# Performance work log

Hardware: AMD Instinct MI355X
Metric: run time of the kernel (lower is better)

## Reference

```python
import jax, jax.numpy as jnp
import numpy as np

L, N, D = 1024, 64, 1024  # seq_len, batch, d_model (= hidden)


def setup_inputs() -> dict:
    key = jax.random.key(0)
    k1, k2, k3 = jax.random.split(key, 3)
    x = jax.random.normal(k1, (L, N, D), dtype=jnp.float32)
    # flax OptimizedLSTMCell params: input kernel (no bias), recurrent kernel + bias,
    # gates packed as [i, f, g, o] along last dim.
    Wi = jax.random.normal(k2, (D, 4 * D), dtype=jnp.float32) / np.float32(np.sqrt(D))
    Wh = jax.random.normal(k3, (D, 4 * D), dtype=jnp.float32) / np.float32(np.sqrt(D))
    b = jnp.zeros((4 * D,), dtype=jnp.float32)
    return {"x": x, "Wi": Wi, "Wh": Wh, "b": b}


def reference(x, Wi, Wh, b):
    # x: [L, N, D]; scan LSTM cell over time axis 0 (matches nn.scan in_axes=0).
    d = Wh.shape[0]
    n = x.shape[1]
    # Input projections have no carry dependency: batch them in one big GEMM.
    xW = jnp.einsum('lnd,df->lnf', x, Wi)  # [L, N, 4D]

    def step(carry, xw_t):
        c, h = carry
        y = xw_t + h @ Wh + b  # [N, 4D]
        i, f, g, o = jnp.split(y, 4, axis=-1)
        i = jax.nn.sigmoid(i)
        f = jax.nn.sigmoid(f)
        g = jnp.tanh(g)
        o = jax.nn.sigmoid(o)
        c_new = f * c + i * g
        h_new = o * jnp.tanh(c_new)
        return (c_new, h_new), h_new

    c0 = jnp.zeros((n, d), dtype=x.dtype)
    h0 = jnp.zeros((n, d), dtype=x.dtype)
    _, hs = jax.lax.scan(step, (c0, h0), xW)
    return hs  # [L, N, D]
```

## Files before the change

kernel.cpp:

```cpp
#include <hip/hip_runtime.h>
#include <stdint.h>

#define LSEQ 1024
#define NB   64
#define DM   1024
#define FOURD 4096

typedef float f32x4 __attribute__((ext_vector_type(4)));
typedef short short8_t __attribute__((ext_vector_type(8)));
typedef __bf16 bf16x8 __attribute__((ext_vector_type(8)));

__device__ __forceinline__ unsigned short f2bf(float f) {
    unsigned int u = __builtin_bit_cast(unsigned int, f);
    u += 0x7fffu + ((u >> 16) & 1u);
    return (unsigned short)(u >> 16);
}

__device__ __forceinline__ f32x4 mfma16(short8_t a, short8_t b, f32x4 c) {
    return __builtin_amdgcn_mfma_f32_16x16x32_bf16(
        __builtin_bit_cast(bf16x8, a), __builtin_bit_cast(bf16x8, b), c, 0, 0, 0);
}

__global__ void init_ws_kernel(unsigned int* __restrict__ p, int n) {
    int i = blockIdx.x * blockDim.x + threadIdx.x;
    int stride = gridDim.x * blockDim.x;
    for (; i < n; i += stride) p[i] = 0u;
}

__global__ void convert_x_kernel(const float4* __restrict__ src, uint4* __restrict__ dst) {
    size_t i = (size_t)blockIdx.x * blockDim.x + threadIdx.x;
    float4 a = src[2 * i];
    float4 b = src[2 * i + 1];
    uint4 r;
    r.x = (unsigned)f2bf(a.x) | ((unsigned)f2bf(a.y) << 16);
    r.y = (unsigned)f2bf(a.z) | ((unsigned)f2bf(a.w) << 16);
    r.z = (unsigned)f2bf(b.x) | ((unsigned)f2bf(b.y) << 16);
    r.w = (unsigned)f2bf(b.z) | ((unsigned)f2bf(b.w) << 16);
    dst[i] = r;
}

__global__ void prep_w_kernel(const float* __restrict__ W,
                              unsigned short* __restrict__ wp) {
    const int fid = blockIdx.x * 256 + threadIdx.x;
    const int lane = fid & 63;
    const int kk = (fid >> 6) & 3;
    const int q  = (fid >> 8) & 3;
    const int ks = (fid >> 10) & 7;
    const int ug = fid >> 13;
    const int k0 = (ks << 7) + (kk << 5) + ((lane >> 4) << 3);
    const int col = (q << 10) + (ug << 4) + (lane & 15);
    short8_t v;
    #pragma unroll
    for (int j = 0; j < 8; ++j)
        v[j] = (short)f2bf(W[(size_t)(k0 + j) * FOURD + col]);
    *(short8_t*)(wp + ((size_t)fid << 3)) = v;
}

#define HL(arr, i, OFFS)                                                        \
    asm volatile("global_load_dwordx4 %0, %1, off offset:" OFFS " sc0 sc1"      \
                 : "=v"(arr[i]) : "v"(hap) : "memory")
#define XL(arr, i, OFFS)                                                        \
    asm volatile("global_load_dwordx4 %0, %1, off offset:" OFFS                 \
                 : "=v"(arr[i]) : "v"(xap) : "memory")
#define WAITV(NSTR)                                          \
    asm volatile("s_waitcnt vmcnt(" NSTR ")" ::: "memory");  \
    __builtin_amdgcn_sched_barrier(0)
#define WAITL()                                              \
    asm volatile("s_waitcnt lgkmcnt(0)" ::: "memory")
#define BARRIER()                                            \
    __builtin_amdgcn_s_barrier();                            \
    asm volatile("" ::: "memory")

__global__ __launch_bounds__(512)
__attribute__((amdgpu_waves_per_eu(2, 2)))
void lstm_scan_kernel(const unsigned short* __restrict__ wip,
                      const unsigned short* __restrict__ whp,
                      const float* __restrict__ bias,
                      const unsigned short* __restrict__ xb,
                      unsigned short* __restrict__ hbuf,
                      unsigned int* __restrict__ flags,
                      float* __restrict__ out)
{
    __shared__ float plds[8][4][16][20];
    const int tid = threadIdx.x;
    const int wg = blockIdx.x;
    const int rg = (wg & 7) >> 1;
    const int ug = (wg >> 3) | ((wg & 1) << 5);
    const int r0 = rg << 4, U0 = ug << 4;
    const int lane = tid & 63, ks = tid >> 6;
    const int la = lane & 15, kseg = lane >> 4;

    short8_t BI[4][4], BH[4][4];
    {
        const unsigned short* wb = wip + (((size_t)(ug << 3) + ks) << 13);
        const unsigned short* hb = whp + (((size_t)(ug << 3) + ks) << 13);
        #pragma unroll
        for (int q = 0; q < 4; ++q)
            #pragma unroll
            for (int kk = 0; kk < 4; ++kk) {
                const unsigned short* p1 = wb + ((((q << 2) + kk) << 6) + lane) * 8;
                const unsigned short* p2 = hb + ((((q << 2) + kk) << 6) + lane) * 8;
                asm volatile("global_load_dwordx4 %0, %1, off"
                             : "=v"(BI[q][kk]) : "v"(p1) : "memory");
                asm volatile("global_load_dwordx4 %0, %1, off"
                             : "=v"(BH[q][kk]) : "v"(p2) : "memory");
            }
        asm volatile("s_waitcnt vmcnt(0)" ::: "memory");
        __builtin_amdgcn_sched_barrier(0);
    }

    const int aoff = (r0 + la) * DM + (ks << 7) + (kseg << 3);

    const int er = tid >> 4, eu = tid & 15;
    const float bI = bias[U0 + eu], bF = bias[1024 + U0 + eu],
                bG = bias[2048 + U0 + eu], bO = bias[3072 + U0 + eu];
    float cst = 0.0f;
    unsigned int* myflag = flags + (rg << 6) + ug;
    const unsigned int* gfp = flags + (rg << 6) + lane;

    short8_t xf[4];
    {
        const unsigned short* xap = xb + aoff;
        XL(xf, 0, "0"); XL(xf, 1, "64"); XL(xf, 2, "128"); XL(xf, 3, "192");
        asm volatile("s_waitcnt vmcnt(0)" ::: "memory");
        __builtin_amdgcn_sched_barrier(0);
    }

    for (int t = 0; t < LSEQ; ++t) {
        if (t && tid < 64) {
            while (true) {
                unsigned int f = __hip_atomic_load(gfp, __ATOMIC_RELAXED,
                                                   __HIP_MEMORY_SCOPE_AGENT);
                if (__all((int)(f >= (unsigned)t))) break;
                __builtin_amdgcn_s_sleep(1);
            }
        }
        BARRIER();

        short8_t hf[4];
        {
            const unsigned short* hap =
                hbuf + (size_t)((t & 1) ^ 1) * (NB * DM) + aoff;
            HL(hf, 0, "0"); HL(hf, 1, "64"); HL(hf, 2, "128"); HL(hf, 3, "192");
        }
        WAITV("4");

        f32x4 acc[4];
        #pragma unroll
        for (int q = 0; q < 4; ++q) acc[q] = (f32x4){0.f, 0.f, 0.f, 0.f};
        #pragma unroll
        for (int kk = 0; kk < 4; ++kk)
            #pragma unroll
            for (int q = 0; q < 4; ++q)
                acc[q] = mfma16(xf[kk], BI[q][kk], acc[q]);

        WAITV("0");

        #pragma unroll
        for (int kk = 0; kk < 4; ++kk)
            #pragma unroll
            for (int q = 0; q < 4; ++q)
                acc[q] = mfma16(hf[kk], BH[q][kk], acc[q]);

        #pragma unroll
        for (int q = 0; q < 4; ++q)
            *(f32x4*)&plds[ks][q][la][kseg << 2] = acc[q];
        WAITL();
        BARRIER();

        float hv = 0.f, hn = 0.f;
        if (tid < 256) {
            float vi = bI, vf = bF, vg = bG, vo = bO;
            #pragma unroll
            for (int s = 0; s < 8; ++s) {
                vi += plds[s][0][eu][er];
                vf += plds[s][1][eu][er];
                vg += plds[s][2][eu][er];
                vo += plds[s][3][eu][er];
            }
            float gi = 1.0f / (1.0f + __expf(-vi));
            float gF = 1.0f / (1.0f + __expf(-vf));
            float gg = 1.0f - 2.0f / (__expf(2.0f * vg) + 1.0f);
            float go = 1.0f / (1.0f + __expf(-vo));
            cst = gF * cst + gi * gg;
            hv = go * (1.0f - 2.0f / (__expf(2.0f * cst) + 1.0f));
            hn = __shfl_xor(hv, 1);

            if (!(eu & 1)) {
                unsigned int hp = (unsigned)f2bf(hv) | ((unsigned)f2bf(hn) << 16);
                unsigned int* hw = (unsigned int*)(hbuf + (size_t)(t & 1) * (NB * DM)
                                                   + (size_t)(r0 + er) * DM + U0 + eu);
                asm volatile("global_store_dword %0, %1, off sc0 sc1"
                             :: "v"(hw), "v"(hp) : "memory");
            }
        }

        {
            const int tn = (t < LSEQ - 1) ? t + 1 : t;
            const unsigned short* xap = xb + (size_t)tn * (NB * DM) + aoff;
            XL(xf, 0, "0"); XL(xf, 1, "64"); XL(xf, 2, "128"); XL(xf, 3, "192");
        }
        WAITV("4");

        BARRIER();

        if (tid == 0)
            __hip_atomic_store(myflag, (unsigned)(t + 1), __ATOMIC_RELAXED,
                               __HIP_MEMORY_SCOPE_AGENT);

        if (tid < 256 && !(eu & 1))
            *(float2*)(out + ((size_t)(t * NB) + r0 + er) * DM + U0 + eu)
                = make_float2(hv, hn);
    }
}

#define HM(arr, i, kk) {                                        \
    short8_t b = *(const short8_t*)(bph + (kk) * 1024);         \
    if ((kk) & 1) acc1 = mfma16(arr[i], b, acc1);               \
    else          acc0 = mfma16(arr[i], b, acc0); }

__global__ __launch_bounds__(256)
void lstm_fallback_kernel(const float* __restrict__ x,
                          const float* __restrict__ Wi,
                          const float* __restrict__ Wh,
                          const float* __restrict__ bias,
                          unsigned short* __restrict__ hbuf,
                          unsigned int* __restrict__ flags,
                          float* __restrict__ out)
{
    __shared__ short Wlds[65536];
    __shared__ float ylds[32 * 33];
    __shared__ float blds[32];

    const int tid  = threadIdx.x;
    const int wgid = blockIdx.x;
    const int g    = wgid >> 7;
    const int ug   = wgid & 127;
    const int U0   = ug << 3;
    const int rowbase = g << 5;

    {
        const int c    = tid & 31;
        const int ct_  = c >> 4;
        const int lb   = c & 15;
        const int gcol = ((c >> 3) << 10) + U0 + (c & 7);
        for (int k = tid >> 5; k < 1024; k += 8) {
            const int lane_ = lb | (((k >> 3) & 3) << 4);
            const int sidx  = (ct_ * 32 + (k >> 5)) * 512 + lane_ * 8 + (k & 7);
            Wlds[sidx]         = (short)f2bf(Wi[(size_t)k * FOURD + gcol]);
            Wlds[sidx + 32768] = (short)f2bf(Wh[(size_t)k * FOURD + gcol]);
        }
        if (tid < 32) blds[tid] = bias[((tid >> 3) << 10) + U0 + (tid & 7)];
    }
    __syncthreads();

    const int lane = tid & 63;
    const int wv   = tid >> 6;
    const int rt   = wv >> 1;
    const int ct   = wv & 1;
    const int arow = rowbase + (rt << 4) + (lane & 15);
    const int kseg = (lane >> 4) << 3;
    const char* bpx = (const char*)Wlds + ct * 32768 + lane * 16;
    const char* bph = (const char*)Wlds + 65536 + ct * 32768 + lane * 16;

    const int er = tid >> 3;
    const int eu = tid & 7;
    const float bI = blds[eu], bF = blds[8 + eu], bG = blds[16 + eu], bO = blds[24 + eu];
    float cstate = 0.0f;
    unsigned int* gflags = flags + (g << 7);

    for (int t = 0; t < LSEQ; ++t) {
        f32x4 acc0 = {0.f, 0.f, 0.f, 0.f};
        f32x4 acc1 = {0.f, 0.f, 0.f, 0.f};

        {
            const float* ap = x + ((size_t)t * NB + arow) * DM + kseg;
            #pragma unroll 4
            for (int kk = 0; kk < 32; ++kk) {
                float4 lo = *(const float4*)(ap + kk * 32);
                float4 hi = *(const float4*)(ap + kk * 32 + 4);
                short8_t a;
                a[0] = (short)f2bf(lo.x); a[1] = (short)f2bf(lo.y);
                a[2] = (short)f2bf(lo.z); a[3] = (short)f2bf(lo.w);
                a[4] = (short)f2bf(hi.x); a[5] = (short)f2bf(hi.y);
                a[6] = (short)f2bf(hi.z); a[7] = (short)f2bf(hi.w);
                short8_t b = *(const short8_t*)(bpx + kk * 1024);
                if (kk & 1) acc1 = mfma16(a, b, acc1);
                else        acc0 = mfma16(a, b, acc0);
            }
        }

        if (t && wv == 0) {
            const unsigned int* fp = gflags + (lane << 1);
            while (true) {
                unsigned int f0 = __hip_atomic_load(fp,     __ATOMIC_RELAXED, __HIP_MEMORY_SCOPE_AGENT);
                unsigned int f1 = __hip_atomic_load(fp + 1, __ATOMIC_RELAXED, __HIP_MEMORY_SCOPE_AGENT);
                int ok = (f0 >= (unsigned)t) && (f1 >= (unsigned)t);
                if (__all(ok)) break;
                __builtin_amdgcn_s_sleep(1);
            }
        }
        __syncthreads();

        {
            const unsigned short* hap =
                hbuf + (size_t)((t & 1) ^ 1) * (NB * DM) + (size_t)arow * DM + kseg;
            short8_t A0[8], A1[8];
            HL(A0,0,"0");    HL(A0,1,"64");   HL(A0,2,"128");  HL(A0,3,"192");
            HL(A0,4,"256");  HL(A0,5,"320");  HL(A0,6,"384");  HL(A0,7,"448");
            HL(A1,0,"512");  HL(A1,1,"576");  HL(A1,2,"640");  HL(A1,3,"704");
            HL(A1,4,"768");  HL(A1,5,"832");  HL(A1,6,"896");  HL(A1,7,"960");
            WAITV("8");
            HM(A0,0,0)  HM(A0,1,1)  HM(A0,2,2)  HM(A0,3,3)
            HM(A0,4,4)  HM(A0,5,5)  HM(A0,6,6)  HM(A0,7,7)
            HL(A0,0,"1024"); HL(A0,1,"1088"); HL(A0,2,"1152"); HL(A0,3,"1216");
            HL(A0,4,"1280"); HL(A0,5,"1344"); HL(A0,6,"1408"); HL(A0,7,"1472");
            WAITV("8");
            HM(A1,0,8)  HM(A1,1,9)  HM(A1,2,10) HM(A1,3,11)
            HM(A1,4,12) HM(A1,5,13) HM(A1,6,14) HM(A1,7,15)
            HL(A1,0,"1536"); HL(A1,1,"1600"); HL(A1,2,"1664"); HL(A1,3,"1728");
            HL(A1,4,"1792"); HL(A1,5,"1856"); HL(A1,6,"1920"); HL(A1,7,"1984");
            WAITV("8");
            HM(A0,0,16) HM(A0,1,17) HM(A0,2,18) HM(A0,3,19)
            HM(A0,4,20) HM(A0,5,21) HM(A0,6,22) HM(A0,7,23)
            WAITV("0");
            HM(A1,0,24) HM(A1,1,25) HM(A1,2,26) HM(A1,3,27)
            HM(A1,4,28) HM(A1,5,29) HM(A1,6,30) HM(A1,7,31)
        }

        {
            f32x4 acc = acc0 + acc1;
            const int rr0 = (rt << 4) + ((lane >> 4) << 2);
            const int c0 = (ct << 4) + (lane & 15);
            #pragma unroll
            for (int j = 0; j < 4; ++j) ylds[(rr0 + j) * 33 + c0] = acc[j];
        }
        __syncthreads();

        {
            const float* yr = ylds + er * 33;
            float vi = yr[eu]      + bI;
            float vf = yr[8 + eu]  + bF;
            float vg = yr[16 + eu] + bG;
            float vo = yr[24 + eu] + bO;
            float gi = 1.0f / (1.0f + __expf(-vi));
            float gF = 1.0f / (1.0f + __expf(-vf));
            float gg = 1.0f - 2.0f / (__expf(2.0f * vg) + 1.0f);
            float go = 1.0f / (1.0f + __expf(-vo));
            cstate = gF * cstate + gi * gg;
            float hv = go * (1.0f - 2.0f / (__expf(2.0f * cstate) + 1.0f));
            float hvn = __shfl_down(hv, 1);
            if ((tid & 1) == 0) {
                const int n = rowbase + er;
                const int d = U0 + eu;
                unsigned int hp = (unsigned)f2bf(hv) | ((unsigned)f2bf(hvn) << 16);
                unsigned int* hw = (unsigned int*)(hbuf + (size_t)(t & 1) * (NB * DM)
                                                   + (size_t)n * DM + d);
                __hip_atomic_store(hw, hp, __ATOMIC_RELAXED, __HIP_MEMORY_SCOPE_AGENT);
                *(float2*)(out + ((size_t)t * NB + n) * DM + d) = make_float2(hv, hvn);
            }
        }
        asm volatile("s_waitcnt vmcnt(0)" ::: "memory");
        __syncthreads();

        if (tid == 0) {
            __hip_atomic_store(gflags + ug, (unsigned)(t + 1),
                               __ATOMIC_RELAXED, __HIP_MEMORY_SCOPE_AGENT);
            asm volatile("s_waitcnt vmcnt(0)" ::: "memory");
        }
    }
}

extern "C" void kernel_launch(void* const* d_in, const int* in_sizes, int n_in,
                              void* d_out, int out_size, void* d_ws, size_t ws_size,
                              hipStream_t stream) {
    (void)in_sizes; (void)n_in; (void)out_size;
    const float* x  = (const float*)d_in[0];
    const float* Wi = (const float*)d_in[1];
    const float* Wh = (const float*)d_in[2];
    const float* b  = (const float*)d_in[3];
    float* out = (float*)d_out;

    char* ws = (char*)d_ws;
    const size_t OFF_HB  = 4096;
    const size_t OFF_WIP = OFF_HB + 262144;
    const size_t OFF_WHP = OFF_WIP + 8388608ull;
    const size_t OFF_XB  = OFF_WHP + 8388608ull;
    const size_t NEED    = OFF_XB + 134217728ull;

    unsigned int*   flags = (unsigned int*)ws;
    unsigned short* hbuf  = (unsigned short*)(ws + OFF_HB);

    init_ws_kernel<<<64, 256, 0, stream>>>((unsigned int*)ws, 66560);

    if (ws_size >= NEED) {
        unsigned short* wip = (unsigned short*)(ws + OFF_WIP);
        unsigned short* whp = (unsigned short*)(ws + OFF_WHP);
        unsigned short* xb  = (unsigned short*)(ws + OFF_XB);
        convert_x_kernel<<<32768, 256, 0, stream>>>((const float4*)x, (uint4*)xb);
        prep_w_kernel<<<2048, 256, 0, stream>>>(Wi, wip);
        prep_w_kernel<<<2048, 256, 0, stream>>>(Wh, whp);
        lstm_scan_kernel<<<256, 512, 0, stream>>>(wip, whp, b, xb, hbuf, flags, out);
    } else {
        lstm_fallback_kernel<<<256, 256, 0, stream>>>(x, Wi, Wh, b, hbuf, flags, out);
    }
}
```

Baseline: 3.825 ms.

## Use per-wave flags for finer-grained cross-block sync and keep weights in AGPRs

Each of the four epilogue waves now publishes its own progress flag right after its h-store completes, instead of one flag per block after a trailing barrier. Every wave polls only the 32 flags for the 128-column K-slice of h it actually reads, which removes the pre-step block barrier and the sleep in the spin loop. The MFMAs become inline asm that takes the weight operand from AGPRs, presumably to relieve VGPR pressure from the 32 resident weight fragments. The risks are memory-ordering correctness with relaxed atomics and more polling traffic from all waves spinning.

```diff
diff --git a/kernel.cpp b/kernel.cpp
--- a/kernel.cpp
+++ b/kernel.cpp
@@ -20,6 +20,10 @@
     return __builtin_amdgcn_mfma_f32_16x16x32_bf16(
         __builtin_bit_cast(bf16x8, a), __builtin_bit_cast(bf16x8, b), c, 0, 0, 0);
 }
+
+#define MFMA_AB(accv, av, bv)                                          \
+    asm volatile("v_mfma_f32_16x16x32_bf16 %0, %1, %2, %0"             \
+                 : "+v"(accv) : "v"(av), "a"(bv))
 
 __global__ void init_ws_kernel(unsigned int* __restrict__ p, int n) {
     int i = blockIdx.x * blockDim.x + threadIdx.x;
@@ -98,15 +102,9 @@
         for (int q = 0; q < 4; ++q)
             #pragma unroll
             for (int kk = 0; kk < 4; ++kk) {
-                const unsigned short* p1 = wb + ((((q << 2) + kk) << 6) + lane) * 8;
-                const unsigned short* p2 = hb + ((((q << 2) + kk) << 6) + lane) * 8;
-                asm volatile("global_load_dwordx4 %0, %1, off"
-                             : "=v"(BI[q][kk]) : "v"(p1) : "memory");
-                asm volatile("global_load_dwordx4 %0, %1, off"
-                             : "=v"(BH[q][kk]) : "v"(p2) : "memory");
-            }
-        asm volatile("s_waitcnt vmcnt(0)" ::: "memory");
-        __builtin_amdgcn_sched_barrier(0);
+                BI[q][kk] = *(const short8_t*)(wb + ((((q << 2) + kk) << 6) + lane) * 8);
+                BH[q][kk] = *(const short8_t*)(hb + ((((q << 2) + kk) << 6) + lane) * 8);
+            }
     }
 
     const int aoff = (r0 + la) * DM + (ks << 7) + (kseg << 3);
@@ -115,27 +113,25 @@
     const float bI = bias[U0 + eu], bF = bias[1024 + U0 + eu],
                 bG = bias[2048 + U0 + eu], bO = bias[3072 + U0 + eu];
     float cst = 0.0f;
-    unsigned int* myflag = flags + (rg << 6) + ug;
-    const unsigned int* gfp = flags + (rg << 6) + lane;
+    unsigned int* wflag = flags + (((rg << 6) + ug) << 2) + ks;
+    const unsigned int* pflag = flags + (((rg << 6) + (ks << 3)) << 2) + (lane & 31);
 
     short8_t xf[4];
     {
         const unsigned short* xap = xb + aoff;
         XL(xf, 0, "0"); XL(xf, 1, "64"); XL(xf, 2, "128"); XL(xf, 3, "192");
-        asm volatile("s_waitcnt vmcnt(0)" ::: "memory");
-        __builtin_amdgcn_sched_barrier(0);
+        WAITV("0");
     }
 
     for (int t = 0; t < LSEQ; ++t) {
-        if (t && tid < 64) {
+        if (t) {
             while (true) {
-                unsigned int f = __hip_atomic_load(gfp, __ATOMIC_RELAXED,
-                                                   __HIP_MEMORY_SCOPE_AGENT);
+                unsigned int f = __hip_atomic_load(pflag, __ATOMIC_RELAXED,
+                                                  __HIP_MEMORY_SCOPE_AGENT);
                 if (__all((int)(f >= (unsigned)t))) break;
-                __builtin_amdgcn_s_sleep(1);
-            }
-        }
-        BARRIER();
+            }
+        }
+        WAITV("0");
 
         short8_t hf[4];
         {
@@ -143,7 +139,6 @@
                 hbuf + (size_t)((t & 1) ^ 1) * (NB * DM) + aoff;
             HL(hf, 0, "0"); HL(hf, 1, "64"); HL(hf, 2, "128"); HL(hf, 3, "192");
         }
-        WAITV("4");
 
         f32x4 acc[4];
         #pragma unroll
@@ -152,7 +147,7 @@
         for (int kk = 0; kk < 4; ++kk)
             #pragma unroll
             for (int q = 0; q < 4; ++q)
-                acc[q] = mfma16(xf[kk], BI[q][kk], acc[q]);
+                MFMA_AB(acc[q], xf[kk], BI[q][kk]);
 
         WAITV("0");
 
@@ -160,7 +155,7 @@
         for (int kk = 0; kk < 4; ++kk)
             #pragma unroll
             for (int q = 0; q < 4; ++q)
-                acc[q] = mfma16(hf[kk], BH[q][kk], acc[q]);
+                MFMA_AB(acc[q], hf[kk], BH[q][kk]);
 
         #pragma unroll
         for (int q = 0; q < 4; ++q)
@@ -193,20 +188,19 @@
                 asm volatile("global_store_dword %0, %1, off sc0 sc1"
                              :: "v"(hw), "v"(hp) : "memory");
             }
-        }
+            asm volatile("s_waitcnt vmcnt(0)" ::: "memory");
+            if ((tid & 63) == 0)
+                __hip_atomic_store(wflag, (unsigned)(t + 1), __ATOMIC_RELAXED,
+                                   __HIP_MEMORY_SCOPE_AGENT);
+        }
+
+        BARRIER();
 
         {
             const int tn = (t < LSEQ - 1) ? t + 1 : t;
             const unsigned short* xap = xb + (size_t)tn * (NB * DM) + aoff;
             XL(xf, 0, "0"); XL(xf, 1, "64"); XL(xf, 2, "128"); XL(xf, 3, "192");
         }
-        WAITV("4");
-
-        BARRIER();
-
-        if (tid == 0)
-            __hip_atomic_store(myflag, (unsigned)(t + 1), __ATOMIC_RELAXED,
-                               __HIP_MEMORY_SCOPE_AGENT);
 
         if (tid < 256 && !(eu & 1))
             *(float2*)(out + ((size_t)(t * NB) + r0 + er) * DM + U0 + eu)
```

Measured after the change: 5.705 ms. 1.49x slower.
